# Kernel tuning notes

Measured on AMD Instinct MI355X. Metric: run time of the kernel, lower is better.

## Reference

```python
import jax, jax.numpy as jnp
import numpy as np

N_NODES = 100000
N_EDGES = 1600000
D_FEAT = 32


def setup_inputs() -> dict:
    key = jax.random.key(0)
    k1, k2, k3 = jax.random.split(key, 3)
    return {
        "x_real": jax.random.normal(k1, (N_NODES, D_FEAT), dtype=jnp.float32),
        "x_imag": jax.random.normal(k2, (N_NODES, D_FEAT), dtype=jnp.float32),
        "edge_index": jax.random.randint(k3, (2, N_EDGES), 0, N_NODES, dtype=jnp.int64),
        "evolution_time": jnp.asarray(0.5, dtype=jnp.float32),
        "diffusion_strength": jnp.asarray(1.0, dtype=jnp.float32),
    }


def reference(x_real, x_imag, edge_index, evolution_time, diffusion_strength):
    eps = 1e-8
    num_nodes = x_real.shape[0]
    x = x_real + 1j * x_imag  # [N, D] complex64

    # add self loops
    loops = jnp.arange(num_nodes, dtype=edge_index.dtype)
    row = jnp.concatenate([edge_index[0], loops])  # [E+N]
    col = jnp.concatenate([edge_index[1], loops])  # [E+N]

    # symmetric degree normalization: deg computed over col (as in source)
    deg = jnp.zeros((num_nodes,), jnp.float32).at[col].add(1.0)
    deg_inv_sqrt = jnp.where(deg > 0, deg ** -0.5, 0.0)
    norm = (deg_inv_sqrt[row] * deg_inv_sqrt[col])[:, None]  # [E+N, 1]

    def propagate(h):
        # gather by col, scale, scatter-add by row
        msgs = h[col] * norm.astype(h.dtype)
        return jnp.zeros_like(h).at[row].add(msgs)

    first_order = propagate(x)
    coeff1 = 1j * (evolution_time * diffusion_strength)
    evolved = x + coeff1 * first_order

    # evolution_order >= 2 (second-order Taylor term)
    second_order = propagate(first_order)
    evolved = evolved + (coeff1 * coeff1) * 0.5 * second_order

    # per-node |psi|^2 weights, normalized to sum to num_nodes
    w = (evolved * jnp.conj(evolved)).real.sum(axis=-1, keepdims=True)  # [N,1]
    s = w.sum()
    w = jnp.where(s > eps, w / s * num_nodes, jnp.ones_like(w))
    return w, evolved
```

## Files before the change

### kernel.cpp

```cpp
#include <hip/hip_runtime.h>
#include <cstdint>
#include <cstddef>


#define TPB 256
#define BSL 128
#define CRANGE 32768
#define SRANGE 32768

typedef _Float16 h2 __attribute__((ext_vector_type(2)));

#if defined(__has_builtin)
#if __has_builtin(__builtin_amdgcn_fdot2)
#define HAS_FDOT2 1
#endif
#endif

__device__ __forceinline__ h2 u2h(uint32_t u) {
    union { uint32_t u; h2 h; } x; x.u = u; return x.h;
}
__device__ __forceinline__ uint32_t h2u(h2 h) {
    union { uint32_t u; h2 h; } x; x.h = h; return x.u;
}
__device__ __forceinline__ uint32_t packh(float re, float im) {
    h2 h; h.x = (_Float16)re; h.y = (_Float16)im; return h2u(h);
}
__device__ __forceinline__ void acc2(uint32_t p, float& aR, float& aI) {
#ifdef HAS_FDOT2
    h2 v = u2h(p);
    h2 LO; LO.x = (_Float16)1.0f; LO.y = (_Float16)0.0f;
    h2 HI; HI.x = (_Float16)0.0f; HI.y = (_Float16)1.0f;
    aR = __builtin_amdgcn_fdot2(v, LO, aR, false);
    aI = __builtin_amdgcn_fdot2(v, HI, aI, false);
#else
    h2 v = u2h(p);
    aR += (float)v.x;
    aI += (float)v.y;
#endif
}
__device__ __forceinline__ void acc4(uint4 p, float (&aR)[4], float (&aI)[4]) {
    acc2(p.x, aR[0], aI[0]);
    acc2(p.y, aR[1], aI[1]);
    acc2(p.z, aR[2], aI[2]);
    acc2(p.w, aR[3], aI[3]);
}

__device__ __forceinline__ int slice_len(int E) {
    return (((E + BSL - 1) / BSL) + 3) & ~3;
}

__global__ void k_cnt2(const int* __restrict__ col, const int* __restrict__ row,
                       int E, int Nq, uint32_t* __restrict__ parts_col,
                       uint32_t* __restrict__ parts_row) {
    __shared__ uint32_t sh[CRANGE / 4];
    int which = blockIdx.x & 1;
    int rb = blockIdx.x >> 1;
    int r = rb / BSL, b = rb % BSL;
    const int* keys = which ? row : col;
    uint32_t*  parts = which ? parts_row : parts_col;
    int rbase = r * CRANGE;
    for (int i = threadIdx.x; i < CRANGE / 4; i += TPB) sh[i] = 0;
    __syncthreads();
    int SL = slice_len(E);
    int s0 = b * SL, s1 = min(E, s0 + SL);
    int n = s1 - s0;
    if (n > 0) {
        const int4* k4 = (const int4*)(keys + s0);
        int n4 = n >> 2;
        for (int j = threadIdx.x; j < n4; j += TPB) {
            int4 v = k4[j];
            int k;
            k = v.x - rbase; if ((unsigned)k < CRANGE) atomicAdd(&sh[k >> 2], 1u << ((k & 3) * 8));
            k = v.y - rbase; if ((unsigned)k < CRANGE) atomicAdd(&sh[k >> 2], 1u << ((k & 3) * 8));
            k = v.z - rbase; if ((unsigned)k < CRANGE) atomicAdd(&sh[k >> 2], 1u << ((k & 3) * 8));
            k = v.w - rbase; if ((unsigned)k < CRANGE) atomicAdd(&sh[k >> 2], 1u << ((k & 3) * 8));
        }
        for (int e = s0 + (n4 << 2) + threadIdx.x; e < s1; e += TPB) {
            int k = keys[e] - rbase;
            if ((unsigned)k < CRANGE) atomicAdd(&sh[k >> 2], 1u << ((k & 3) * 8));
        }
    }
    __syncthreads();
    int wbase = rbase >> 2;
    for (int i = threadIdx.x; i < CRANGE / 4; i += TPB) {
        int w = wbase + i;
        if (w < Nq) parts[(size_t)b * Nq + w] = sh[i];
    }
}

__global__ void k_discol(const uint32_t* __restrict__ parts, int Nq, int N,
                         float* __restrict__ dis) {
    int w = blockIdx.x * blockDim.x + threadIdx.x;
    if (w >= Nq) return;
    int c0 = 0, c1 = 0, c2 = 0, c3 = 0;
    for (int b = 0; b < BSL; ++b) {
        uint32_t v = parts[(size_t)b * Nq + w];
        c0 += v & 255u; c1 += (v >> 8) & 255u; c2 += (v >> 16) & 255u; c3 += v >> 24;
    }
    int n = 4 * w;
    if (n < N)     dis[n]     = rsqrtf((float)c0 + 1.0f);
    if (n + 1 < N) dis[n + 1] = rsqrtf((float)c1 + 1.0f);
    if (n + 2 < N) dis[n + 2] = rsqrtf((float)c2 + 1.0f);
    if (n + 3 < N) dis[n + 3] = rsqrtf((float)c3 + 1.0f);
}

__global__ void k_redrow(const uint32_t* __restrict__ parts, int Nq, int N,
                         uint32_t* __restrict__ sliceoff_w,
                         int* __restrict__ rowcnt) {
    int w = blockIdx.x * blockDim.x + threadIdx.x;
    if (w >= Nq) return;
    int c0 = 0, c1 = 0, c2 = 0, c3 = 0;
    for (int b = 0; b < BSL; ++b) {
        uint32_t v = parts[(size_t)b * Nq + w];
        sliceoff_w[(size_t)b * Nq + w] =
            (uint32_t)c0 | ((uint32_t)c1 << 8) | ((uint32_t)c2 << 16) |
            ((uint32_t)c3 << 24);
        c0 += v & 255u; c1 += (v >> 8) & 255u; c2 += (v >> 16) & 255u; c3 += v >> 24;
    }
    int n = 4 * w;
    if (n < N)     rowcnt[n]     = c0;
    if (n + 1 < N) rowcnt[n + 1] = c1;
    if (n + 2 < N) rowcnt[n + 2] = c2;
    if (n + 3 < N) rowcnt[n + 3] = c3;
}

__global__ void k_scan1(const int* __restrict__ in, int* __restrict__ out,
                        int* __restrict__ partials, int N) {
    __shared__ int sh[256];
    int t = threadIdx.x;
    int base = blockIdx.x * 1024 + t * 4;
    int v0 = (base + 0 < N) ? in[base + 0] : 0;
    int v1 = (base + 1 < N) ? in[base + 1] : 0;
    int v2 = (base + 2 < N) ? in[base + 2] : 0;
    int v3 = (base + 3 < N) ? in[base + 3] : 0;
    int s = v0 + v1 + v2 + v3;
    sh[t] = s;
    __syncthreads();
    for (int off = 1; off < 256; off <<= 1) {
        int add = (t >= off) ? sh[t - off] : 0;
        __syncthreads();
        sh[t] += add;
        __syncthreads();
    }
    int excl = sh[t] - s;
    if (base + 0 < N) out[base + 0] = excl;
    excl += v0;
    if (base + 1 < N) out[base + 1] = excl;
    excl += v1;
    if (base + 2 < N) out[base + 2] = excl;
    excl += v2;
    if (base + 3 < N) out[base + 3] = excl;
    if (t == 255) partials[blockIdx.x] = sh[255];
}

__global__ void k_scan2(int* __restrict__ partials, int nb) {
    if (threadIdx.x == 0 && blockIdx.x == 0) {
        int acc = 0;
        for (int i = 0; i < nb; ++i) { int v = partials[i]; partials[i] = acc; acc += v; }
    }
}

__global__ void k_scan3(int* __restrict__ out, const int* __restrict__ partials,
                        int N, int E) {
    int i = blockIdx.x * blockDim.x + threadIdx.x;
    if (i < N) out[i] += partials[i >> 10];
    if (i == 0) out[N] = E;
}

__global__ void k_scatter2(const int* __restrict__ row, const int* __restrict__ col,
                           int E, int N, int Nq, const int* __restrict__ rowptr,
                           const uint32_t* __restrict__ sliceoff_w,
                           int* __restrict__ ecol) {
    __shared__ uint32_t cur[SRANGE / 4];
    int r = blockIdx.x / BSL, b = blockIdx.x % BSL;
    int rbase = r * SRANGE;
    int wb = rbase >> 2;
    for (int i = threadIdx.x; i < SRANGE / 4; i += TPB)
        cur[i] = (wb + i < Nq) ? sliceoff_w[(size_t)b * Nq + wb + i] : 0u;
    __syncthreads();
    int SL = slice_len(E);
    int s0 = b * SL, s1 = min(E, s0 + SL);
    int n = s1 - s0;
    if (n <= 0) return;
    const int4* r4 = (const int4*)(row + s0);
    const int4* c4 = (const int4*)(col + s0);
    int n4 = n >> 2;
    for (int j = threadIdx.x; j < n4; j += TPB) {
        int4 rv = r4[j];
        int4 cv = c4[j];
        #pragma unroll
        for (int q = 0; q < 4; ++q) {
            int rr = ((const int*)&rv)[q] - rbase;
            if ((unsigned)rr < SRANGE) {
                uint32_t old = atomicAdd(&cur[rr >> 2], 1u << ((rr & 3) * 8));
                int off = (int)((old >> ((rr & 3) * 8)) & 0xFFu);
                ecol[rowptr[rbase + rr] + off] = ((const int*)&cv)[q];
            }
        }
    }
    for (int e = s0 + (n4 << 2) + threadIdx.x; e < s1; e += TPB) {
        int rr = row[e] - rbase;
        if ((unsigned)rr < SRANGE) {
            uint32_t old = atomicAdd(&cur[rr >> 2], 1u << ((rr & 3) * 8));
            int off = (int)((old >> ((rr & 3) * 8)) & 0xFFu);
            ecol[rowptr[rbase + rr] + off] = col[e];
        }
    }
}

__global__ void k_pack(const float* __restrict__ xr, const float* __restrict__ xi,
                       const float* __restrict__ dis, uint32_t* __restrict__ xds,
                       int N) {
    int i = blockIdx.x * blockDim.x + threadIdx.x;
    if (i < N * 32) {
        int n = i >> 5, k = i & 31, s = k >> 3, dd = k & 7;
        float dg = dis[n];
        xds[((size_t)s * N + n) * 8 + dd] = packh(xr[i] * dg, xi[i] * dg);
    }
}

__device__ __forceinline__ void edge_accum4(const int* __restrict__ ecol,
                                            const uint4* __restrict__ hb4,
                                            int beg, int end, int epos, int half,
                                            float (&aR)[4], float (&aI)[4]) {
    int base = beg;
    for (; base + 16 <= end; base += 16) {
        int c0 = ecol[base + epos];
        int c1 = ecol[base + epos + 4];
        int c2 = ecol[base + epos + 8];
        int c3 = ecol[base + epos + 12];
        uint4 p0 = hb4[(size_t)c0 * 2 + half];
        uint4 p1 = hb4[(size_t)c1 * 2 + half];
        uint4 p2 = hb4[(size_t)c2 * 2 + half];
        uint4 p3 = hb4[(size_t)c3 * 2 + half];
        acc4(p0, aR, aI); acc4(p1, aR, aI);
        acc4(p2, aR, aI); acc4(p3, aR, aI);
    }
    if (base + 8 <= end) {
        int c0 = ecol[base + epos];
        int c1 = ecol[base + epos + 4];
        uint4 p0 = hb4[(size_t)c0 * 2 + half];
        uint4 p1 = hb4[(size_t)c1 * 2 + half];
        acc4(p0, aR, aI); acc4(p1, aR, aI);
        base += 8;
    }
    int rem = end - base;
    if (epos < rem) {
        int c = ecol[base + epos];
        uint4 p = hb4[(size_t)c * 2 + half];
        acc4(p, aR, aI);
    }
    if (epos + 4 < rem) {
        int c = ecol[base + epos + 4];
        uint4 p = hb4[(size_t)c * 2 + half];
        acc4(p, aR, aI);
    }
}

__device__ __forceinline__ void reduce8(float (&aR)[4], float (&aI)[4]) {
    #pragma unroll
    for (int d = 0; d < 4; ++d) {
        aR[d] += __shfl_xor(aR[d], 2, 8);
        aI[d] += __shfl_xor(aI[d], 2, 8);
        aR[d] += __shfl_xor(aR[d], 4, 8);
        aI[d] += __shfl_xor(aI[d], 4, 8);
    }
}

__global__ void k_p1(const int* __restrict__ rowptr, const int* __restrict__ ecol,
                     const float* __restrict__ dis, const uint32_t* __restrict__ xds,
                     uint32_t* __restrict__ fods, int N) {
    int s   = blockIdx.x & 3;
    int nb  = blockIdx.x >> 2;
    int r   = nb * 32 + (threadIdx.x >> 3);
    int sub = threadIdx.x & 7;
    int half = sub & 1, epos = sub >> 1;
    if (r >= N) return;
    const uint4* hb4 = (const uint4*)(xds + (size_t)s * N * 8);
    int beg = rowptr[r], end = rowptr[r + 1];
    float dg = dis[r];
    float aR[4] = {0.f, 0.f, 0.f, 0.f}, aI[4] = {0.f, 0.f, 0.f, 0.f};
    edge_accum4(ecol, hb4, beg, end, epos, half, aR, aI);
    reduce8(aR, aI);
    acc4(hb4[(size_t)r * 2 + half], aR, aI);
    if (epos == 0) {
        float dg2 = dg * dg;
        uint4 fd;
        fd.x = packh(dg2 * aR[0], dg2 * aI[0]);
        fd.y = packh(dg2 * aR[1], dg2 * aI[1]);
        fd.z = packh(dg2 * aR[2], dg2 * aI[2]);
        fd.w = packh(dg2 * aR[3], dg2 * aI[3]);
        ((uint4*)(fods + (size_t)s * N * 8))[(size_t)r * 2 + half] = fd;
    }
}

__global__ void k_p2(const int* __restrict__ rowptr, const int* __restrict__ ecol,
                     const float* __restrict__ dis, const uint32_t* __restrict__ fods,
                     const float* __restrict__ tptr, const float* __restrict__ dptr,
                     uint32_t* __restrict__ delta, int N) {
    int s   = blockIdx.x & 3;
    int nb  = blockIdx.x >> 2;
    int r   = nb * 32 + (threadIdx.x >> 3);
    int sub = threadIdx.x & 7;
    int half = sub & 1, epos = sub >> 1;
    if (r >= N) return;
    const uint4* hb4 = (const uint4*)(fods + (size_t)s * N * 8);
    int beg = rowptr[r], end = rowptr[r + 1];
    float dg = dis[r];
    float aR[4] = {0.f, 0.f, 0.f, 0.f}, aI[4] = {0.f, 0.f, 0.f, 0.f};
    edge_accum4(ecol, hb4, beg, end, epos, half, aR, aI);
    reduce8(aR, aI);
    uint4 fv4 = hb4[(size_t)r * 2 + half];
    acc4(fv4, aR, aI);
    if (epos == 0) {
        float c1  = tptr[0] * dptr[0];
        float c2h = 0.5f * c1 * c1;
        float inv = 1.0f / dg;
        uint32_t fu[4] = {fv4.x, fv4.y, fv4.z, fv4.w};
        uint4 dlt;
        uint32_t dv[4];
        #pragma unroll
        for (int d = 0; d < 4; ++d) {
            float soR = dg * aR[d], soI = dg * aI[d];
            h2 f = u2h(fu[d]);
            float foR = (float)f.x * inv, foI = (float)f.y * inv;
            dv[d] = packh(-c1 * foI - c2h * soR, c1 * foR - c2h * soI);
        }
        dlt.x = dv[0]; dlt.y = dv[1]; dlt.z = dv[2]; dlt.w = dv[3];
        ((uint4*)(delta + (size_t)s * N * 8))[(size_t)r * 2 + half] = dlt;
    }
}

__global__ void k_final(const float* __restrict__ xr, const float* __restrict__ xi,
                        const uint32_t* __restrict__ delta, float* __restrict__ out,
                        int N, int interleaved, float* __restrict__ partials2) {
    int t = blockIdx.x * blockDim.x + threadIdx.x;
    int n = t >> 2, s = t & 3;
    float wsum = 0.f;
    if (n < N) {
        const uint4* dp = (const uint4*)(delta + ((size_t)s * N + n) * 8);
        uint4 d0 = dp[0], d1 = dp[1];
        size_t ib = (size_t)n * 32 + (size_t)s * 8;
        const float4* xr4 = (const float4*)(xr + ib);
        const float4* xi4 = (const float4*)(xi + ib);
        float4 a0 = xr4[0], a1 = xr4[1];
        float4 b0 = xi4[0], b1 = xi4[1];
        uint32_t dv[8] = {d0.x, d0.y, d0.z, d0.w, d1.x, d1.y, d1.z, d1.w};
        float ar[8] = {a0.x, a0.y, a0.z, a0.w, a1.x, a1.y, a1.z, a1.w};
        float ai[8] = {b0.x, b0.y, b0.z, b0.w, b1.x, b1.y, b1.z, b1.w};
        float er[8], ei[8];
        #pragma unroll
        for (int k = 0; k < 8; ++k) {
            h2 d = u2h(dv[k]);
            er[k] = ar[k] + (float)d.x;
            ei[k] = ai[k] + (float)d.y;
            wsum += er[k] * er[k] + ei[k] * ei[k];
        }
        if (interleaved) {
            float4* op = (float4*)(out + N + 2 * ib);
            op[0] = make_float4(er[0], ei[0], er[1], ei[1]);
            op[1] = make_float4(er[2], ei[2], er[3], ei[3]);
            op[2] = make_float4(er[4], ei[4], er[5], ei[5]);
            op[3] = make_float4(er[6], ei[6], er[7], ei[7]);
        } else {
            float4* op = (float4*)(out + N + ib);
            op[0] = make_float4(er[0], er[1], er[2], er[3]);
            op[1] = make_float4(er[4], er[5], er[6], er[7]);
        }
    }
    float nodesum = wsum;
    nodesum += __shfl_xor(nodesum, 1, 4);
    nodesum += __shfl_xor(nodesum, 2, 4);
    if (n < N && s == 0) out[n] = nodesum;
    float bv = wsum;
    #pragma unroll
    for (int off = 32; off; off >>= 1) bv += __shfl_xor(bv, off, 64);
    __shared__ float ls[TPB / 64];
    if ((threadIdx.x & 63) == 0) ls[threadIdx.x >> 6] = bv;
    __syncthreads();
    if (threadIdx.x == 0) {
        float bs = 0.f;
        #pragma unroll
        for (int i = 0; i < TPB / 64; ++i) bs += ls[i];
        partials2[blockIdx.x] = bs;
    }
}

__global__ void k_sum(const float* __restrict__ partials2, int nb,
                      float* __restrict__ S) {
    float acc = 0.f;
    for (int i = threadIdx.x; i < nb; i += blockDim.x) acc += partials2[i];
    #pragma unroll
    for (int off = 32; off; off >>= 1) acc += __shfl_xor(acc, off, 64);
    __shared__ float ls[TPB / 64];
    if ((threadIdx.x & 63) == 0) ls[threadIdx.x >> 6] = acc;
    __syncthreads();
    if (threadIdx.x == 0) {
        float s = 0.f;
        #pragma unroll
        for (int i = 0; i < TPB / 64; ++i) s += ls[i];
        *S = s;
    }
}

__global__ void k_norm(float* __restrict__ w, int N, const float* __restrict__ S) {
    int i = blockIdx.x * blockDim.x + threadIdx.x;
    if (i >= N) return;
    float s = *S;
    w[i] = (s > 1e-8f) ? w[i] * ((float)N / s) : 1.0f;
}

extern "C" void kernel_launch(void* const* d_in, const int* in_sizes, int n_in,
                              void* d_out, int out_size, void* d_ws, size_t ws_size,
                              hipStream_t stream) {
    const float* xr   = (const float*)d_in[0];
    const float* xi   = (const float*)d_in[1];
    const int*   eidx = (const int*)d_in[2];
    const float* tptr = (const float*)d_in[3];
    const float* dptr = (const float*)d_in[4];

    const int N = in_sizes[0] / 32;
    const int E = in_sizes[2] / 2;
    const int* row = eidx;
    const int* col = eidx + E;
    const long long ND = (long long)N * 32;
    const int Nq  = (N + 3) / 4;
    const int NB  = (N + 1023) / 1024;
    const int NBK = (N + 31) / 32;
    const int NFB = (int)((ND / 8 + TPB - 1) / TPB);
    const int NCR = (N + CRANGE - 1) / CRANGE;
    const int NSR = (N + SRANGE - 1) / SRANGE;
    const int pgrid = 4 * NBK;

    size_t o = 0;
    auto alloc = [&](size_t words) {
        o = (o + 3) & ~(size_t)3;
        size_t r = o; o += words; return r;
    };
    size_t slab = (size_t)BSL * Nq;
    size_t slab_row = slab < (size_t)ND ? (size_t)ND : slab;
    size_t slab_col = slab < (size_t)E ? (size_t)E : slab;
    uint32_t* wsw = (uint32_t*)d_ws;
    uint32_t* parts_row  = wsw + alloc(slab_row);
    uint32_t* parts_col  = wsw + alloc(slab_col);
    uint32_t* sliceoff_w = wsw + alloc(slab);
    int*      rowcnt     = (int*)(wsw + alloc(N));
    int*      rowptr     = (int*)(wsw + alloc(N + 1));
    int*      partials   = (int*)(wsw + alloc(NB + 2));
    float*    dis        = (float*)(wsw + alloc(N));
    uint32_t* xds        = wsw + alloc(ND);
    uint32_t* fods       = wsw + alloc(ND);
    float*    partials2  = (float*)(wsw + alloc(NFB));
    float*    S          = (float*)(wsw + alloc(1));
    uint32_t* delta      = parts_row;
    int*      ecol       = (int*)parts_col;

    int interleaved = (out_size >= (int)(N + 2 * ND)) ? 1 : 0;
    float* out = (float*)d_out;

    k_cnt2<<<NCR * BSL * 2, TPB, 0, stream>>>(col, row, E, Nq, parts_col, parts_row);
    k_discol<<<(Nq + TPB - 1) / TPB, TPB, 0, stream>>>(parts_col, Nq, N, dis);
    k_redrow<<<(Nq + TPB - 1) / TPB, TPB, 0, stream>>>(parts_row, Nq, N,
                                                       sliceoff_w, rowcnt);
    k_scan1<<<NB, TPB, 0, stream>>>(rowcnt, rowptr, partials, N);
    k_scan2<<<1, 64, 0, stream>>>(partials, NB);
    k_scan3<<<(N + TPB - 1) / TPB, TPB, 0, stream>>>(rowptr, partials, N, E);
    k_scatter2<<<NSR * BSL, TPB, 0, stream>>>(row, col, E, N, Nq, rowptr,
                                              sliceoff_w, ecol);

    k_pack<<<(int)((ND + TPB - 1) / TPB), TPB, 0, stream>>>(xr, xi, dis, xds, N);
    k_p1<<<pgrid, TPB, 0, stream>>>(rowptr, ecol, dis, xds, fods, N);
    k_p2<<<pgrid, TPB, 0, stream>>>(rowptr, ecol, dis, fods, tptr, dptr, delta, N);
    k_final<<<NFB, TPB, 0, stream>>>(xr, xi, delta, out, N, interleaved, partials2);
    k_sum<<<1, TPB, 0, stream>>>(partials2, NFB, S);
    k_norm<<<(N + TPB - 1) / TPB, TPB, 0, stream>>>(out, N, S);
}
```

Baseline: 196.1 us.

## Switch gather to full-row node-major fp16 layout, one 8-lane group per row

Replaces the 4-slice feature layout (each row processed by 4 blocks, each reading 32-byte half-slices with edge-split lanes and shuffle reduction) with a node-major packed layout where 8 lanes each load 16 bytes of a node's full 128-byte fp16 row for every edge. Each gathered row then becomes one contiguous 128-byte access instead of four separate 32-byte accesses spread across slices. The shuffle reduction is dropped, and the edge index list is read once per row instead of once per slice. Every lane now walks all edges of its row serially, which gives less parallelism per edge for high-degree rows. Workspace alignment is also raised to 128 bytes.

```diff
diff --git a/kernel.cpp b/kernel.cpp
--- a/kernel.cpp
+++ b/kernel.cpp
@@ -209,126 +209,89 @@
 }
 
 __global__ void k_pack(const float* __restrict__ xr, const float* __restrict__ xi,
-                       const float* __restrict__ dis, uint32_t* __restrict__ xds,
+                       const float* __restrict__ dis, uint32_t* __restrict__ xd,
                        int N) {
     int i = blockIdx.x * blockDim.x + threadIdx.x;
     if (i < N * 32) {
-        int n = i >> 5, k = i & 31, s = k >> 3, dd = k & 7;
-        float dg = dis[n];
-        xds[((size_t)s * N + n) * 8 + dd] = packh(xr[i] * dg, xi[i] * dg);
-    }
-}
-
-__device__ __forceinline__ void edge_accum4(const int* __restrict__ ecol,
-                                            const uint4* __restrict__ hb4,
-                                            int beg, int end, int epos, int half,
-                                            float (&aR)[4], float (&aI)[4]) {
+        float dg = dis[i >> 5];
+        xd[i] = packh(xr[i] * dg, xi[i] * dg);
+    }
+}
+
+__device__ __forceinline__ void edge_accum_row(const int* __restrict__ ecol,
+                                               const uint4* __restrict__ h4,
+                                               int beg, int end, int sub,
+                                               float (&aR)[4], float (&aI)[4]) {
     int base = beg;
-    for (; base + 16 <= end; base += 16) {
-        int c0 = ecol[base + epos];
-        int c1 = ecol[base + epos + 4];
-        int c2 = ecol[base + epos + 8];
-        int c3 = ecol[base + epos + 12];
-        uint4 p0 = hb4[(size_t)c0 * 2 + half];
-        uint4 p1 = hb4[(size_t)c1 * 2 + half];
-        uint4 p2 = hb4[(size_t)c2 * 2 + half];
-        uint4 p3 = hb4[(size_t)c3 * 2 + half];
+    for (; base + 4 <= end; base += 4) {
+        int c0 = ecol[base + 0];
+        int c1 = ecol[base + 1];
+        int c2 = ecol[base + 2];
+        int c3 = ecol[base + 3];
+        uint4 p0 = h4[(size_t)c0 * 8 + sub];
+        uint4 p1 = h4[(size_t)c1 * 8 + sub];
+        uint4 p2 = h4[(size_t)c2 * 8 + sub];
+        uint4 p3 = h4[(size_t)c3 * 8 + sub];
         acc4(p0, aR, aI); acc4(p1, aR, aI);
         acc4(p2, aR, aI); acc4(p3, aR, aI);
     }
-    if (base + 8 <= end) {
-        int c0 = ecol[base + epos];
-        int c1 = ecol[base + epos + 4];
-        uint4 p0 = hb4[(size_t)c0 * 2 + half];
-        uint4 p1 = hb4[(size_t)c1 * 2 + half];
-        acc4(p0, aR, aI); acc4(p1, aR, aI);
-        base += 8;
-    }
-    int rem = end - base;
-    if (epos < rem) {
-        int c = ecol[base + epos];
-        uint4 p = hb4[(size_t)c * 2 + half];
+    for (; base < end; ++base) {
+        int c = ecol[base];
+        uint4 p = h4[(size_t)c * 8 + sub];
         acc4(p, aR, aI);
     }
-    if (epos + 4 < rem) {
-        int c = ecol[base + epos + 4];
-        uint4 p = hb4[(size_t)c * 2 + half];
-        acc4(p, aR, aI);
-    }
-}
-
-__device__ __forceinline__ void reduce8(float (&aR)[4], float (&aI)[4]) {
-    #pragma unroll
-    for (int d = 0; d < 4; ++d) {
-        aR[d] += __shfl_xor(aR[d], 2, 8);
-        aI[d] += __shfl_xor(aI[d], 2, 8);
-        aR[d] += __shfl_xor(aR[d], 4, 8);
-        aI[d] += __shfl_xor(aI[d], 4, 8);
-    }
 }
 
 __global__ void k_p1(const int* __restrict__ rowptr, const int* __restrict__ ecol,
-                     const float* __restrict__ dis, const uint32_t* __restrict__ xds,
+                     const float* __restrict__ dis, const uint32_t* __restrict__ xd,
                      uint32_t* __restrict__ fods, int N) {
-    int s   = blockIdx.x & 3;
-    int nb  = blockIdx.x >> 2;
-    int r   = nb * 32 + (threadIdx.x >> 3);
+    int r   = blockIdx.x * 32 + (threadIdx.x >> 3);
     int sub = threadIdx.x & 7;
-    int half = sub & 1, epos = sub >> 1;
     if (r >= N) return;
-    const uint4* hb4 = (const uint4*)(xds + (size_t)s * N * 8);
+    const uint4* h4 = (const uint4*)xd;
     int beg = rowptr[r], end = rowptr[r + 1];
     float dg = dis[r];
     float aR[4] = {0.f, 0.f, 0.f, 0.f}, aI[4] = {0.f, 0.f, 0.f, 0.f};
-    edge_accum4(ecol, hb4, beg, end, epos, half, aR, aI);
-    reduce8(aR, aI);
-    acc4(hb4[(size_t)r * 2 + half], aR, aI);
-    if (epos == 0) {
-        float dg2 = dg * dg;
-        uint4 fd;
-        fd.x = packh(dg2 * aR[0], dg2 * aI[0]);
-        fd.y = packh(dg2 * aR[1], dg2 * aI[1]);
-        fd.z = packh(dg2 * aR[2], dg2 * aI[2]);
-        fd.w = packh(dg2 * aR[3], dg2 * aI[3]);
-        ((uint4*)(fods + (size_t)s * N * 8))[(size_t)r * 2 + half] = fd;
-    }
+    edge_accum_row(ecol, h4, beg, end, sub, aR, aI);
+    acc4(h4[(size_t)r * 8 + sub], aR, aI);
+    float dg2 = dg * dg;
+    uint4 fd;
+    fd.x = packh(dg2 * aR[0], dg2 * aI[0]);
+    fd.y = packh(dg2 * aR[1], dg2 * aI[1]);
+    fd.z = packh(dg2 * aR[2], dg2 * aI[2]);
+    fd.w = packh(dg2 * aR[3], dg2 * aI[3]);
+    ((uint4*)fods)[(size_t)r * 8 + sub] = fd;
 }
 
 __global__ void k_p2(const int* __restrict__ rowptr, const int* __restrict__ ecol,
                      const float* __restrict__ dis, const uint32_t* __restrict__ fods,
                      const float* __restrict__ tptr, const float* __restrict__ dptr,
                      uint32_t* __restrict__ delta, int N) {
-    int s   = blockIdx.x & 3;
-    int nb  = blockIdx.x >> 2;
-    int r   = nb * 32 + (threadIdx.x >> 3);
+    int r   = blockIdx.x * 32 + (threadIdx.x >> 3);
     int sub = threadIdx.x & 7;
-    int half = sub & 1, epos = sub >> 1;
     if (r >= N) return;
-    const uint4* hb4 = (const uint4*)(fods + (size_t)s * N * 8);
+    const uint4* h4 = (const uint4*)fods;
     int beg = rowptr[r], end = rowptr[r + 1];
     float dg = dis[r];
     float aR[4] = {0.f, 0.f, 0.f, 0.f}, aI[4] = {0.f, 0.f, 0.f, 0.f};
-    edge_accum4(ecol, hb4, beg, end, epos, half, aR, aI);
-    reduce8(aR, aI);
-    uint4 fv4 = hb4[(size_t)r * 2 + half];
+    edge_accum_row(ecol, h4, beg, end, sub, aR, aI);
+    uint4 fv4 = h4[(size_t)r * 8 + sub];
     acc4(fv4, aR, aI);
-    if (epos == 0) {
-        float c1  = tptr[0] * dptr[0];
-        float c2h = 0.5f * c1 * c1;
-        float inv = 1.0f / dg;
-        uint32_t fu[4] = {fv4.x, fv4.y, fv4.z, fv4.w};
-        uint4 dlt;
-        uint32_t dv[4];
-        #pragma unroll
-        for (int d = 0; d < 4; ++d) {
-            float soR = dg * aR[d], soI = dg * aI[d];
-            h2 f = u2h(fu[d]);
-            float foR = (float)f.x * inv, foI = (float)f.y * inv;
-            dv[d] = packh(-c1 * foI - c2h * soR, c1 * foR - c2h * soI);
-        }
-        dlt.x = dv[0]; dlt.y = dv[1]; dlt.z = dv[2]; dlt.w = dv[3];
-        ((uint4*)(delta + (size_t)s * N * 8))[(size_t)r * 2 + half] = dlt;
-    }
+    float c1  = tptr[0] * dptr[0];
+    float c2h = 0.5f * c1 * c1;
+    float inv = 1.0f / dg;
+    uint32_t fu[4] = {fv4.x, fv4.y, fv4.z, fv4.w};
+    uint4 dlt;
+    uint32_t dv[4];
+    #pragma unroll
+    for (int d = 0; d < 4; ++d) {
+        float soR = dg * aR[d], soI = dg * aI[d];
+        h2 f = u2h(fu[d]);
+        float foR = (float)f.x * inv, foI = (float)f.y * inv;
+        dv[d] = packh(-c1 * foI - c2h * soR, c1 * foR - c2h * soI);
+    }
+    dlt.x = dv[0]; dlt.y = dv[1]; dlt.z = dv[2]; dlt.w = dv[3];
+    ((uint4*)delta)[(size_t)r * 8 + sub] = dlt;
 }
 
 __global__ void k_final(const float* __restrict__ xr, const float* __restrict__ xi,
@@ -338,9 +301,9 @@
     int n = t >> 2, s = t & 3;
     float wsum = 0.f;
     if (n < N) {
-        const uint4* dp = (const uint4*)(delta + ((size_t)s * N + n) * 8);
+        size_t ib = (size_t)n * 32 + (size_t)s * 8;
+        const uint4* dp = (const uint4*)(delta + ib);
         uint4 d0 = dp[0], d1 = dp[1];
-        size_t ib = (size_t)n * 32 + (size_t)s * 8;
         const float4* xr4 = (const float4*)(xr + ib);
         const float4* xi4 = (const float4*)(xi + ib);
         float4 a0 = xr4[0], a1 = xr4[1];
@@ -430,11 +393,10 @@
     const int NFB = (int)((ND / 8 + TPB - 1) / TPB);
     const int NCR = (N + CRANGE - 1) / CRANGE;
     const int NSR = (N + SRANGE - 1) / SRANGE;
-    const int pgrid = 4 * NBK;
 
     size_t o = 0;
     auto alloc = [&](size_t words) {
-        o = (o + 3) & ~(size_t)3;
+        o = (o + 31) & ~(size_t)31;
         size_t r = o; o += words; return r;
     };
     size_t slab = (size_t)BSL * Nq;
@@ -448,7 +410,7 @@
     int*      rowptr     = (int*)(wsw + alloc(N + 1));
     int*      partials   = (int*)(wsw + alloc(NB + 2));
     float*    dis        = (float*)(wsw + alloc(N));
-    uint32_t* xds        = wsw + alloc(ND);
+    uint32_t* xd         = wsw + alloc(ND);
     uint32_t* fods       = wsw + alloc(ND);
     float*    partials2  = (float*)(wsw + alloc(NFB));
     float*    S          = (float*)(wsw + alloc(1));
@@ -468,9 +430,9 @@
     k_scatter2<<<NSR * BSL, TPB, 0, stream>>>(row, col, E, N, Nq, rowptr,
                                               sliceoff_w, ecol);
 
-    k_pack<<<(int)((ND + TPB - 1) / TPB), TPB, 0, stream>>>(xr, xi, dis, xds, N);
-    k_p1<<<pgrid, TPB, 0, stream>>>(rowptr, ecol, dis, xds, fods, N);
-    k_p2<<<pgrid, TPB, 0, stream>>>(rowptr, ecol, dis, fods, tptr, dptr, delta, N);
+    k_pack<<<(int)((ND + TPB - 1) / TPB), TPB, 0, stream>>>(xr, xi, dis, xd, N);
+    k_p1<<<NBK, TPB, 0, stream>>>(rowptr, ecol, dis, xd, fods, N);
+    k_p2<<<NBK, TPB, 0, stream>>>(rowptr, ecol, dis, fods, tptr, dptr, delta, N);
     k_final<<<NFB, TPB, 0, stream>>>(xr, xi, delta, out, N, interleaved, partials2);
     k_sum<<<1, TPB, 0, stream>>>(partials2, NFB, S);
     k_norm<<<(N + TPB - 1) / TPB, TPB, 0, stream>>>(out, N, S);
```

After: 174.9 us. -10.8%, faster.
